# Kernel optimization log

Hardware: AMD Instinct MI355X
Metric: run time of the kernel (lower is better)

## Reference

```python
import jax, jax.numpy as jnp
import numpy as np

C = 64      # in_channels
CO = 64     # out_channels
S = 256     # spatial size
K = 3       # kernel size (identity-preserving)
P = 1       # padding = (K-1)//2
L = S * S


def unfold(x):
    # torch.nn.Unfold(kernel_size=K, padding=P): (1,C,S,S) -> (1, C*K*K, L)
    # ordering: channel slowest, then kernel row-major, spatial L row-major
    xp = jnp.pad(x, ((0, 0), (0, 0), (P, P), (P, P)))
    pats = [xp[:, :, i:i + S, j:j + S] for i in range(K) for j in range(K)]
    u = jnp.stack(pats, axis=2)  # (1, C, K*K, S, S)
    return u.reshape(x.shape[0], C * K * K, L)


def fold(u):
    # torch.nn.Fold: overlap-add inverse of unfold. (1, C*K*K, L) -> (1, C, S, S)
    u = u.reshape(-1, C, K, K, S, S)
    out = jnp.zeros((u.shape[0], C, S + 2 * P, S + 2 * P), dtype=u.dtype)
    for i in range(K):
        for j in range(K):
            out = out.at[:, :, i:i + S, j:j + S].add(u[:, :, i, j])
    return out[:, :, P:P + S, P:P + S]


def setup_inputs() -> dict:
    key = jax.random.key(0)
    k1, k2, k3 = jax.random.split(key, 3)
    x = jax.random.uniform(k1, (1, C, S, S), dtype=jnp.float32)  # activations in [0,1]
    weight = jax.random.uniform(k2, (1, C * K * K, L), dtype=jnp.float32)  # unfolded reverb weight
    # xavier_normal_ for (C, CO): std = sqrt(2/(fan_in+fan_out))
    conv = jax.random.normal(k3, (C, CO), dtype=jnp.float32) * np.float32(np.sqrt(2.0 / (C + CO)))
    return {"x": x, "weight": weight, "conv": conv}


def reference(x, weight, conv):
    h1 = weight * unfold(x)          # (1, C*K*K, L) elementwise
    h2 = fold(h1).reshape(C, L)      # overlap-add, then flatten spatial
    y = jnp.einsum('cl,co->ol', h2, conv)  # channel mixing: (CO, L)
    return y.reshape(1, CO, S, S)
```

## Files before the change

kernel.cpp:

```cpp
#include <hip/hip_runtime.h>


#define SS 256
#define CH 64
#define LL (SS * SS)

__global__ __launch_bounds__(1024, 4) void reverb_fused(
    const float* __restrict__ xin,
    const float* __restrict__ w,
    const float* __restrict__ conv,
    float* __restrict__ out)
{
    __shared__ float h2[CH][SS];
    __shared__ float cv[CH][CH];

    const int t    = threadIdx.x;
    const int y    = blockIdx.x;
    const int lane = t & 63;
    const int wv   = t >> 6;

    reinterpret_cast<float4*>(&cv[0][0])[t] =
        reinterpret_cast<const float4*>(conv)[t];

    const int px = lane << 2;
#pragma unroll
    for (int cc = 0; cc < 4; ++cc) {
        const int c = (wv << 2) + cc;
        const float4 xv = *reinterpret_cast<const float4*>(
            xin + (size_t)c * LL + (size_t)y * SS + px);
        float s0 = 0.f, s1 = 0.f, s2 = 0.f, s3 = 0.f;
        const float* wc = w + (size_t)c * 9 * LL;
#pragma unroll
        for (int i = 0; i < 3; ++i) {
            const int r = y + 1 - i;
            if ((unsigned)r < (unsigned)SS) {
                const float* base = wc + (size_t)(i * 3) * LL + (size_t)r * SS + px;
                const float4 v0 = *reinterpret_cast<const float4*>(base);
                const float4 v1 = *reinterpret_cast<const float4*>(base + LL);
                const float4 v2 = *reinterpret_cast<const float4*>(base + 2 * LL);
                s0 += v1.x; s1 += v1.y; s2 += v1.z; s3 += v1.w;
                float nx = __shfl_down(v0.x, 1);
                if (lane == 63) nx = 0.f;
                s0 += v0.y; s1 += v0.z; s2 += v0.w; s3 += nx;
                float pv = __shfl_up(v2.w, 1);
                if (lane == 0) pv = 0.f;
                s0 += pv; s1 += v2.x; s2 += v2.y; s3 += v2.z;
            }
        }
        float4 hr;
        hr.x = xv.x * s0; hr.y = xv.y * s1; hr.z = xv.z * s2; hr.w = xv.w * s3;
        *reinterpret_cast<float4*>(&h2[c][px]) = hr;
    }
    __syncthreads();

    const int p4 = (t & 63) << 2;
    const int o0 = (t >> 6) << 2;

    float4 acc[4];
#pragma unroll
    for (int oo = 0; oo < 4; ++oo) acc[oo] = make_float4(0.f, 0.f, 0.f, 0.f);

#pragma unroll 8
    for (int c = 0; c < CH; ++c) {
        const float4 hv = *reinterpret_cast<const float4*>(&h2[c][p4]);
        const float4 cw = *reinterpret_cast<const float4*>(&cv[c][o0]);
        acc[0].x += cw.x * hv.x; acc[0].y += cw.x * hv.y;
        acc[0].z += cw.x * hv.z; acc[0].w += cw.x * hv.w;
        acc[1].x += cw.y * hv.x; acc[1].y += cw.y * hv.y;
        acc[1].z += cw.y * hv.z; acc[1].w += cw.y * hv.w;
        acc[2].x += cw.z * hv.x; acc[2].y += cw.z * hv.y;
        acc[2].z += cw.z * hv.z; acc[2].w += cw.z * hv.w;
        acc[3].x += cw.w * hv.x; acc[3].y += cw.w * hv.y;
        acc[3].z += cw.w * hv.z; acc[3].w += cw.w * hv.w;
    }

    float* op = out + (size_t)o0 * LL + (size_t)y * SS + p4;
#pragma unroll
    for (int oo = 0; oo < 4; ++oo)
        *reinterpret_cast<float4*>(op + (size_t)oo * LL) = acc[oo];
}

extern "C" void kernel_launch(void* const* d_in, const int* in_sizes, int n_in,
                              void* d_out, int out_size, void* d_ws, size_t ws_size,
                              hipStream_t stream) {
    const float* x    = (const float*)d_in[0];
    const float* w    = (const float*)d_in[1];
    const float* conv = (const float*)d_in[2];
    float* out        = (float*)d_out;

    reverb_fused<<<dim3(256), dim3(1024), 0, stream>>>(x, w, conv, out);
}
```

Measured before the change: 232.5 us.

## Split fused kernel into fine-grained h2 pass and separate channel-mix kernel

Replaces the single fused kernel, which ran only 256 blocks of 1024 threads, with two kernels. The first computes the weighted overlap-add per (row, channel) over 4096 small blocks and writes h2 to workspace. The second does the 64x64 channel mix over 128-pixel tiles with 8 outputs per thread. The aim is more parallelism so the large weight stream (about 150MB) is read with better latency hiding. The cost is a 16MB round trip of h2 through global memory plus a second launch; the old fused path is kept as a fallback when the workspace is too small.

```diff
diff --git a/kernel.cpp b/kernel.cpp
--- a/kernel.cpp
+++ b/kernel.cpp
@@ -5,29 +5,118 @@
 #define CH 64
 #define LL (SS * SS)
 
-__global__ __launch_bounds__(1024, 4) void reverb_fused(
+__global__ __launch_bounds__(256, 4) void reverb_h2(
     const float* __restrict__ xin,
     const float* __restrict__ w,
+    float* __restrict__ h2)
+{
+    const int t    = threadIdx.x;
+    const int lane = t & 63;
+    const int wv   = t >> 6;
+    const int task = (blockIdx.x << 2) + wv;
+    const int y    = task >> 6;
+    const int c    = task & 63;
+    const int px   = lane << 2;
+
+    const float4 xv = *reinterpret_cast<const float4*>(
+        xin + (size_t)c * LL + (size_t)y * SS + px);
+
+    float s0 = 0.f, s1 = 0.f, s2 = 0.f, s3 = 0.f;
+    const float* wc = w + (size_t)c * 9 * LL;
+#pragma unroll
+    for (int i = 0; i < 3; ++i) {
+        const int r = y + 1 - i;
+        if ((unsigned)r < (unsigned)SS) {
+            const float* base = wc + (size_t)(i * 3) * LL + (size_t)r * SS + px;
+            const float4 v0 = *reinterpret_cast<const float4*>(base);
+            const float4 v1 = *reinterpret_cast<const float4*>(base + LL);
+            const float4 v2 = *reinterpret_cast<const float4*>(base + 2 * LL);
+            s0 += v1.x; s1 += v1.y; s2 += v1.z; s3 += v1.w;
+            float nx = __shfl_down(v0.x, 1);
+            if (lane == 63) nx = 0.f;
+            s0 += v0.y; s1 += v0.z; s2 += v0.w; s3 += nx;
+            float pv = __shfl_up(v2.w, 1);
+            if (lane == 0) pv = 0.f;
+            s0 += pv; s1 += v2.x; s2 += v2.y; s3 += v2.z;
+        }
+    }
+    float4 hr;
+    hr.x = xv.x * s0; hr.y = xv.y * s1; hr.z = xv.z * s2; hr.w = xv.w * s3;
+    *reinterpret_cast<float4*>(h2 + (size_t)c * LL + (size_t)y * SS + px) = hr;
+}
+
+__global__ __launch_bounds__(256, 2) void reverb_mix(
+    const float* __restrict__ h2,
     const float* __restrict__ conv,
     float* __restrict__ out)
 {
+    __shared__ float hs[CH][128];
+    __shared__ float cv[CH][CH];
+
+    const int t   = threadIdx.x;
+    const int px0 = blockIdx.x << 7;
+
+    {
+        const float4* g4 = reinterpret_cast<const float4*>(conv);
+        float4* s4 = reinterpret_cast<float4*>(&cv[0][0]);
+#pragma unroll
+        for (int k = 0; k < 4; ++k)
+            s4[k * 256 + t] = g4[k * 256 + t];
+    }
+    {
+        float4* s4 = reinterpret_cast<float4*>(&hs[0][0]);
+#pragma unroll
+        for (int k = 0; k < 8; ++k) {
+            const int f  = k * 256 + t;
+            const int r  = f >> 5;
+            const int c4 = f & 31;
+            s4[f] = *reinterpret_cast<const float4*>(
+                h2 + (size_t)r * LL + px0 + (c4 << 2));
+        }
+    }
+    __syncthreads();
+
+    const int q  = t & 31;
+    const int o0 = (t >> 5) << 3;
+
+    float4 acc[8];
+#pragma unroll
+    for (int oo = 0; oo < 8; ++oo) acc[oo] = make_float4(0.f, 0.f, 0.f, 0.f);
+
+#pragma unroll 8
+    for (int c = 0; c < CH; ++c) {
+        const float4 hv = *reinterpret_cast<const float4*>(&hs[c][q << 2]);
+        const float4 ca = *reinterpret_cast<const float4*>(&cv[c][o0]);
+        const float4 cb = *reinterpret_cast<const float4*>(&cv[c][o0 + 4]);
+        const float cw[8] = {ca.x, ca.y, ca.z, ca.w, cb.x, cb.y, cb.z, cb.w};
+#pragma unroll
+        for (int oo = 0; oo < 8; ++oo) {
+            acc[oo].x += cw[oo] * hv.x;
+            acc[oo].y += cw[oo] * hv.y;
+            acc[oo].z += cw[oo] * hv.z;
+            acc[oo].w += cw[oo] * hv.w;
+        }
+    }
+
+    float* op = out + px0 + (q << 2);
+#pragma unroll
+    for (int oo = 0; oo < 8; ++oo)
+        *reinterpret_cast<float4*>(op + (size_t)(o0 + oo) * LL) = acc[oo];
+}
+
+__global__ __launch_bounds__(1024, 4) void reverb_fused(
+    const float* __restrict__ xin, const float* __restrict__ w,
+    const float* __restrict__ conv, float* __restrict__ out)
+{
     __shared__ float h2[CH][SS];
     __shared__ float cv[CH][CH];
-
-    const int t    = threadIdx.x;
-    const int y    = blockIdx.x;
-    const int lane = t & 63;
-    const int wv   = t >> 6;
-
-    reinterpret_cast<float4*>(&cv[0][0])[t] =
-        reinterpret_cast<const float4*>(conv)[t];
-
+    const int t = threadIdx.x, y = blockIdx.x, lane = t & 63, wv = t >> 6;
+    reinterpret_cast<float4*>(&cv[0][0])[t] = reinterpret_cast<const float4*>(conv)[t];
     const int px = lane << 2;
 #pragma unroll
     for (int cc = 0; cc < 4; ++cc) {
         const int c = (wv << 2) + cc;
-        const float4 xv = *reinterpret_cast<const float4*>(
-            xin + (size_t)c * LL + (size_t)y * SS + px);
+        const float4 xv = *reinterpret_cast<const float4*>(xin + (size_t)c * LL + (size_t)y * SS + px);
         float s0 = 0.f, s1 = 0.f, s2 = 0.f, s3 = 0.f;
         const float* wc = w + (size_t)c * 9 * LL;
 #pragma unroll
@@ -39,41 +128,29 @@
                 const float4 v1 = *reinterpret_cast<const float4*>(base + LL);
                 const float4 v2 = *reinterpret_cast<const float4*>(base + 2 * LL);
                 s0 += v1.x; s1 += v1.y; s2 += v1.z; s3 += v1.w;
-                float nx = __shfl_down(v0.x, 1);
-                if (lane == 63) nx = 0.f;
+                float nx = __shfl_down(v0.x, 1); if (lane == 63) nx = 0.f;
                 s0 += v0.y; s1 += v0.z; s2 += v0.w; s3 += nx;
-                float pv = __shfl_up(v2.w, 1);
-                if (lane == 0) pv = 0.f;
+                float pv = __shfl_up(v2.w, 1);   if (lane == 0) pv = 0.f;
                 s0 += pv; s1 += v2.x; s2 += v2.y; s3 += v2.z;
             }
         }
-        float4 hr;
-        hr.x = xv.x * s0; hr.y = xv.y * s1; hr.z = xv.z * s2; hr.w = xv.w * s3;
+        float4 hr; hr.x = xv.x * s0; hr.y = xv.y * s1; hr.z = xv.z * s2; hr.w = xv.w * s3;
         *reinterpret_cast<float4*>(&h2[c][px]) = hr;
     }
     __syncthreads();
-
-    const int p4 = (t & 63) << 2;
-    const int o0 = (t >> 6) << 2;
-
+    const int p4 = (t & 63) << 2, o0 = (t >> 6) << 2;
     float4 acc[4];
 #pragma unroll
     for (int oo = 0; oo < 4; ++oo) acc[oo] = make_float4(0.f, 0.f, 0.f, 0.f);
-
 #pragma unroll 8
     for (int c = 0; c < CH; ++c) {
         const float4 hv = *reinterpret_cast<const float4*>(&h2[c][p4]);
         const float4 cw = *reinterpret_cast<const float4*>(&cv[c][o0]);
-        acc[0].x += cw.x * hv.x; acc[0].y += cw.x * hv.y;
-        acc[0].z += cw.x * hv.z; acc[0].w += cw.x * hv.w;
-        acc[1].x += cw.y * hv.x; acc[1].y += cw.y * hv.y;
-        acc[1].z += cw.y * hv.z; acc[1].w += cw.y * hv.w;
-        acc[2].x += cw.z * hv.x; acc[2].y += cw.z * hv.y;
-        acc[2].z += cw.z * hv.z; acc[2].w += cw.z * hv.w;
-        acc[3].x += cw.w * hv.x; acc[3].y += cw.w * hv.y;
-        acc[3].z += cw.w * hv.z; acc[3].w += cw.w * hv.w;
+        acc[0].x += cw.x * hv.x; acc[0].y += cw.x * hv.y; acc[0].z += cw.x * hv.z; acc[0].w += cw.x * hv.w;
+        acc[1].x += cw.y * hv.x; acc[1].y += cw.y * hv.y; acc[1].z += cw.y * hv.z; acc[1].w += cw.y * hv.w;
+        acc[2].x += cw.z * hv.x; acc[2].y += cw.z * hv.y; acc[2].z += cw.z * hv.z; acc[2].w += cw.z * hv.w;
+        acc[3].x += cw.w * hv.x; acc[3].y += cw.w * hv.y; acc[3].z += cw.w * hv.z; acc[3].w += cw.w * hv.w;
     }
-
     float* op = out + (size_t)o0 * LL + (size_t)y * SS + p4;
 #pragma unroll
     for (int oo = 0; oo < 4; ++oo)
@@ -88,5 +165,12 @@
     const float* conv = (const float*)d_in[2];
     float* out        = (float*)d_out;
 
-    reverb_fused<<<dim3(256), dim3(1024), 0, stream>>>(x, w, conv, out);
+    const size_t h2_bytes = (size_t)CH * LL * sizeof(float);
+    if (ws_size >= h2_bytes) {
+        float* h2 = (float*)d_ws;
+        reverb_h2 <<<dim3(4096), dim3(256), 0, stream>>>(x, w, h2);
+        reverb_mix<<<dim3(512),  dim3(256), 0, stream>>>(h2, conv, out);
+    } else {
+        reverb_fused<<<dim3(256), dim3(1024), 0, stream>>>(x, w, conv, out);
+    }
 }
```

New measurement: 242.8 us. 4.4% more time.
